# Performance work log

Measured on AMD Instinct MI355X. Metric: run time of the kernel, lower is better.

Reference implementation:

```python
import jax, jax.numpy as jnp
import numpy as np

H = 768
R = 24


def setup_inputs() -> dict:
    key = jax.random.key(0)
    ks = jax.random.split(key, 9)
    B, S = 4, 256
    hidden = jax.random.normal(ks[0], (B, S, H), dtype=jnp.float32)
    # ConcatHandshaking fc: Linear(2H -> H); torch weight shape (out,in)=(H,2H)
    fc_w = jax.random.normal(ks[1], (H, 2 * H), dtype=jnp.float32) * (1.0 / np.sqrt(2 * H))
    fc_b = jnp.zeros((H,), dtype=jnp.float32)
    # h2t: Linear(H -> 2)
    h2t_w = jax.random.normal(ks[2], (2, H), dtype=jnp.float32) * (1.0 / np.sqrt(H))
    h2t_b = jnp.zeros((2,), dtype=jnp.float32)
    # h2h / t2t TaggingProjector: R independent Linear(H -> 3), batched as (R,3,H)
    h2h_w = jax.random.normal(ks[3], (R, 3, H), dtype=jnp.float32) * (1.0 / np.sqrt(H))
    h2h_b = jnp.zeros((R, 3), dtype=jnp.float32)
    t2t_w = jax.random.normal(ks[4], (R, 3, H), dtype=jnp.float32) * (1.0 / np.sqrt(H))
    t2t_b = jnp.zeros((R, 3), dtype=jnp.float32)
    return {
        "hidden": hidden,
        "fc_w": fc_w, "fc_b": fc_b,
        "h2t_w": h2t_w, "h2t_b": h2t_b,
        "h2h_w": h2h_w, "h2h_b": h2h_b,
        "t2t_w": t2t_w, "t2t_b": t2t_b,
    }


def _handshaking(hidden, fc_w, fc_b):
    # hidden: (B, S, H). Pairs (i, j) with i <= j in row-major (torch loop) order.
    S = hidden.shape[1]
    idx_i, idx_j = jnp.triu_indices(S)  # each (P,), P = S(S+1)/2
    # concat([h_i, h_j]) @ W^T == h_i @ Wl^T + h_j @ Wr^T  (avoids (B,P,2H) buffer)
    Wl = fc_w[:, :H]  # (H, H)
    Wr = fc_w[:, H:]  # (H, H)
    left = jnp.einsum('bsh,oh->bso', hidden, Wl)   # (B, S, H)
    right = jnp.einsum('bsh,oh->bso', hidden, Wr)  # (B, S, H)
    hs = jnp.tanh(left[:, idx_i, :] + right[:, idx_j, :] + fc_b)  # (B, P, H)
    return hs


def reference(hidden, fc_w, fc_b, h2t_w, h2t_b, h2h_w, h2h_b, t2t_w, t2t_b):
    hs = _handshaking(hidden, fc_w, fc_b)  # (B, P, H)
    # h2t: plain Linear(H->2), logits (no softmax in original)
    h2t = jnp.einsum('bph,oh->bpo', hs, h2t_w) + h2t_b  # (B, P, 2)
    # TaggingProjector: batched per-relation Linear(H->3), then softmax over tags
    h2h = jax.nn.softmax(jnp.einsum('bph,rth->brpt', hs, h2h_w) + h2h_b[None, :, None, :], axis=-1)
    t2t = jax.nn.softmax(jnp.einsum('bph,rth->brpt', hs, t2t_w) + t2t_b[None, :, None, :], axis=-1)
    return (h2t, h2h, t2t)
```

## Files before the change

### kernel.cpp

```cpp
#include <hip/hip_runtime.h>
#include <hip/hip_bf16.h>

#define H 768
#define SEQ 256
#define NPAIR 32896
#define NOUTP 160
#define OFF_H2H 263168u
#define OFF_T2T 9737216u

#define N_BPK 122880
#define N_FCW 1179648

typedef short bf16x8 __attribute__((ext_vector_type(8)));
typedef float f32x4 __attribute__((ext_vector_type(4)));

__device__ __forceinline__ float tanh_act(float x) {
    float e = __builtin_amdgcn_exp2f(x * 2.8853900817779268f);
    return fmaf(-2.0f, __builtin_amdgcn_rcpf(e + 1.0f), 1.0f);
}
__device__ __forceinline__ float bf_lo(int w){ return __uint_as_float(((unsigned)w) << 16); }
__device__ __forceinline__ float bf_hi(int w){ return __uint_as_float(((unsigned)w) & 0xffff0000u); }
__device__ __forceinline__ int cvtpk(float lo, float hi) {
    int r;
    asm("v_cvt_pk_bf16_f32 %0, %1, %2" : "=v"(r) : "v"(lo), "v"(hi));
    return r;
}
__device__ __forceinline__ unsigned short bf16r(float x){
    unsigned int u = __float_as_uint(x);
    u += 0x7fffu + ((u >> 16) & 1u);
    return (unsigned short)(u >> 16);
}

__device__ __forceinline__ int row_start(int i) { return i * SEQ - (i * (i - 1)) / 2; }
__device__ __forceinline__ void pair_ij(int p, int& oi, int& oj) {
    double disc = 263169.0 - 8.0 * (double)p;
    int i = (int)((513.0 - sqrt(disc)) * 0.5);
    if (i > 0 && row_start(i) > p) --i;
    while (row_start(i + 1) <= p) ++i;
    oi = i;
    oj = i + (p - row_start(i));
}

__global__ __launch_bounds__(256) void pack_kernel(
    const float* __restrict__ h2t_w, const float* __restrict__ h2h_w,
    const float* __restrict__ t2t_w, const float* __restrict__ h2t_b,
    const float* __restrict__ h2h_b, const float* __restrict__ t2t_b,
    const float* __restrict__ fc_w,
    unsigned short* __restrict__ Bpk, unsigned short* __restrict__ fcwb,
    float* __restrict__ bc)
{
    int idx = blockIdx.x * 256 + threadIdx.x;
    if (idx < N_BPK) {
        int j = idx & 7, lane = (idx >> 3) & 63, rest = idx >> 9;
        int f = rest % 10, k32 = rest / 10;
        int n = f * 16 + (lane & 15);
        int k = k32 * 32 + ((lane >> 4) << 3) + j;
        float v = 0.f;
        if (n < 2)        v = h2t_w[n * H + k];
        else if (n < 74)  v = h2h_w[(n - 2) * H + k];
        else if (n < 146) v = t2t_w[(n - 74) * H + k];
        Bpk[idx] = bf16r(v);
    } else if (idx < N_BPK + N_FCW) {
        int q = idx - N_BPK;
        int n = q / H, k = q % H;
        float v = (n < H) ? fc_w[(size_t)n * 2 * H + k]
                          : fc_w[(size_t)(n - H) * 2 * H + H + k];
        fcwb[q] = bf16r(v);
    } else if (idx < N_BPK + N_FCW + NOUTP) {
        int q = idx - N_BPK - N_FCW;
        float v = 0.f;
        if (q < 2)        v = h2t_b[q];
        else if (q < 74)  v = h2h_b[q - 2];
        else if (q < 146) v = t2t_b[q - 74];
        bc[q] = v;
    }
}

__global__ __launch_bounds__(256, 2) void lr_mfma(
    const float* __restrict__ hidden, const unsigned short* __restrict__ fcwb,
    const float* __restrict__ fc_b,
    unsigned short* __restrict__ LB, unsigned short* __restrict__ RB)
{
    __shared__ __align__(16) char sm[24576];
    const int tid = threadIdx.x, l = tid & 63, w = tid >> 6;
    const int wm = w >> 1, wn = w & 1;
    const int m0 = blockIdx.x * 64, n0 = blockIdx.y * 128;
    f32x4 acc[2][4] = {};
    for (int c = 0; c < 12; ++c) {
        const int k0 = c * 64;
        #pragma unroll
        for (int it = 0; it < 2; ++it) {
            int idx = tid + it * 256;
            int row = idx >> 3, k8 = idx & 7;
            const float4* src = reinterpret_cast<const float4*>(hidden + (size_t)(m0 + row) * H + k0 + k8 * 8);
            float4 a = src[0], bq = src[1];
            int4 st;
            st.x = cvtpk(a.x, a.y);  st.y = cvtpk(a.z, a.w);
            st.z = cvtpk(bq.x, bq.y); st.w = cvtpk(bq.z, bq.w);
            *reinterpret_cast<int4*>(sm + row * 128 + ((k8 * 16) ^ ((row & 7) << 4))) = st;
        }
        #pragma unroll
        for (int it = 0; it < 4; ++it) {
            int idx = tid + it * 256;
            int row = idx >> 3, k8 = idx & 7;
            *reinterpret_cast<int4*>(sm + 8192 + row * 128 + ((k8 * 16) ^ ((row & 7) << 4))) =
                *reinterpret_cast<const int4*>(fcwb + (size_t)(n0 + row) * H + k0 + k8 * 8);
        }
        __syncthreads();
        #pragma unroll
        for (int kk = 0; kk < 2; ++kk) {
            const int sl = kk * 4 + (l >> 4);
            const int swz = (l & 7) << 4;
            bf16x8 af[2], bfr[4];
            #pragma unroll
            for (int a = 0; a < 2; ++a) {
                int row = 32 * wm + 16 * a + (l & 15);
                af[a] = *reinterpret_cast<const bf16x8*>(sm + row * 128 + ((sl * 16) ^ swz));
            }
            #pragma unroll
            for (int f = 0; f < 4; ++f) {
                int row = 64 * wn + 16 * f + (l & 15);
                bfr[f] = *reinterpret_cast<const bf16x8*>(sm + 8192 + row * 128 + ((sl * 16) ^ swz));
            }
            #pragma unroll
            for (int a = 0; a < 2; ++a)
                #pragma unroll
                for (int f = 0; f < 4; ++f)
                    acc[a][f] = __builtin_amdgcn_mfma_f32_16x16x32_bf16(af[a], bfr[f], acc[a][f], 0, 0, 0);
        }
        __syncthreads();
    }
    #pragma unroll
    for (int a = 0; a < 2; ++a)
        #pragma unroll
        for (int f = 0; f < 4; ++f)
            #pragma unroll
            for (int r = 0; r < 4; ++r) {
                int row = m0 + 32 * wm + 16 * a + 4 * (l >> 4) + r;
                int col = n0 + 64 * wn + 16 * f + (l & 15);
                float v = acc[a][f][r];
                if (n0 < H) LB[(size_t)row * H + col] = bf16r(v + fc_b[col]);
                else        RB[(size_t)row * H + (col - H)] = bf16r(v);
            }
}

__device__ __forceinline__ void stage_row(char* dst, const unsigned short* lp, const unsigned short* rp) {
    int4 lv = *reinterpret_cast<const int4*>(lp);
    int4 rv = *reinterpret_cast<const int4*>(rp);
    int4 st;
    st.x = cvtpk(tanh_act(bf_lo(lv.x) + bf_lo(rv.x)), tanh_act(bf_hi(lv.x) + bf_hi(rv.x)));
    st.y = cvtpk(tanh_act(bf_lo(lv.y) + bf_lo(rv.y)), tanh_act(bf_hi(lv.y) + bf_hi(rv.y)));
    st.z = cvtpk(tanh_act(bf_lo(lv.z) + bf_lo(rv.z)), tanh_act(bf_hi(lv.z) + bf_hi(rv.z)));
    st.w = cvtpk(tanh_act(bf_lo(lv.w) + bf_lo(rv.w)), tanh_act(bf_hi(lv.w) + bf_hi(rv.w)));
    *reinterpret_cast<int4*>(dst) = st;
}

__global__ __launch_bounds__(512, 4) void pair_mfma(
    const unsigned short* __restrict__ LB, const unsigned short* __restrict__ RB,
    const unsigned short* __restrict__ Bpk, const float* __restrict__ bc,
    float* __restrict__ out)
{
    __shared__ __align__(16) char sm[38528];
    int*   iOf  = reinterpret_cast<int*>(sm + 36864);
    int*   jOf  = reinterpret_cast<int*>(sm + 37376);
    float* bc_s = reinterpret_cast<float*>(sm + 37888);

    const int tid = threadIdx.x, l = tid & 63, w = tid >> 6;
    const int wm = w >> 1, wn = w & 1;
    const int b = blockIdx.y, p0 = blockIdx.x * 128;

    if (tid < 128) {
        int i, j; pair_ij(p0 + tid, i, j);
        iOf[tid] = i * H; jOf[tid] = j * H;
    }
    if (tid < NOUTP) bc_s[tid] = bc[tid];
    __syncthreads();

    const unsigned short* LBb = LB + (size_t)b * SEQ * H;
    const unsigned short* RBb = RB + (size_t)b * SEQ * H;
    const int qA = tid >> 3, k8 = tid & 7;
    const unsigned short* lpA = LBb + iOf[qA] + k8 * 8;
    const unsigned short* rpA = RBb + jOf[qA] + k8 * 8;
    const unsigned short* lpB = LBb + iOf[qA + 64] + k8 * 8;
    const unsigned short* rpB = RBb + jOf[qA + 64] + k8 * 8;
    char* stA = sm + qA * 128 + ((k8 * 16) ^ ((qA & 7) << 4));
    char* stB = stA + 64 * 128;

    f32x4 acc[2][5] = {};
    const int4* bsrc = reinterpret_cast<const int4*>(Bpk);
    int4* bdst = reinterpret_cast<int4*>(sm + 16384);

    for (int c = 0; c < 12; ++c) {
        const int k0 = c * 64;
        stage_row(stA, lpA + k0, rpA + k0);
        stage_row(stB, lpB + k0, rpB + k0);
        bdst[tid]        = bsrc[c * 1280 + tid];
        bdst[tid + 512]  = bsrc[c * 1280 + tid + 512];
        if (tid < 256) bdst[tid + 1024] = bsrc[c * 1280 + tid + 1024];
        __syncthreads();
        #pragma unroll
        for (int kk = 0; kk < 2; ++kk) {
            const int sl16 = (kk * 4 + (l >> 4)) * 16;
            const int swz = (l & 7) << 4;
            bf16x8 af[2];
            #pragma unroll
            for (int m = 0; m < 2; ++m) {
                int row = 32 * wm + 16 * m + (l & 15);
                af[m] = *reinterpret_cast<const bf16x8*>(sm + row * 128 + (sl16 ^ swz));
            }
            #pragma unroll
            for (int f = 0; f < 5; ++f) {
                bf16x8 bfr = *reinterpret_cast<const bf16x8*>(
                    sm + 16384 + ((kk * 10 + wn * 5 + f) * 64 + l) * 16);
                #pragma unroll
                for (int m = 0; m < 2; ++m)
                    acc[m][f] = __builtin_amdgcn_mfma_f32_16x16x32_bf16(af[m], bfr, acc[m][f], 0, 0, 0);
            }
        }
        __syncthreads();
    }

    float* scw = reinterpret_cast<float*>(sm);
    for (int s = 0; s < 4; ++s) {
        if (wm == s) {
            #pragma unroll
            for (int m = 0; m < 2; ++m)
                #pragma unroll
                for (int f = 0; f < 5; ++f)
                    #pragma unroll
                    for (int r = 0; r < 4; ++r) {
                        int rl = 16 * m + 4 * (l >> 4) + r;
                        int col = 80 * wn + 16 * f + (l & 15);
                        scw[rl * 172 + col] = acc[m][f][r];
                    }
        }
        __syncthreads();
        if (tid < 64) {
            int rl = tid >> 1, tt = tid & 1;
            int p = p0 + 32 * s + rl;
            out[((size_t)b * NPAIR + p) * 2 + tt] = scw[rl * 172 + tt] + bc_s[tt];
        }
        #pragma unroll
        for (int it = 0; it < 3; ++it) {
            int item = it * 512 + tid;
            int rl = item & 31, rr = item >> 5;
            int ob = 2 + rr * 3;
            float l0 = scw[rl * 172 + ob + 0] + bc_s[ob + 0];
            float l1 = scw[rl * 172 + ob + 1] + bc_s[ob + 1];
            float l2 = scw[rl * 172 + ob + 2] + bc_s[ob + 2];
            float mx = fmaxf(l0, fmaxf(l1, l2));
            float e0 = __expf(l0 - mx), e1 = __expf(l1 - mx), e2 = __expf(l2 - mx);
            float inv = __fdividef(1.0f, e0 + e1 + e2);
            int p = p0 + 32 * s + rl;
            size_t base = (rr < 24)
                ? (size_t)OFF_H2H + ((size_t)(b * 24 + rr) * NPAIR + p) * 3
                : (size_t)OFF_T2T + ((size_t)(b * 24 + rr - 24) * NPAIR + p) * 3;
            out[base + 0] = e0 * inv;
            out[base + 1] = e1 * inv;
            out[base + 2] = e2 * inv;
        }
        __syncthreads();
    }
}

extern "C" void kernel_launch(void* const* d_in, const int* in_sizes, int n_in,
                              void* d_out, int out_size, void* d_ws, size_t ws_size,
                              hipStream_t stream) {
    const float* hidden = (const float*)d_in[0];
    const float* fc_w   = (const float*)d_in[1];
    const float* fc_b   = (const float*)d_in[2];
    const float* h2t_w  = (const float*)d_in[3];
    const float* h2t_b  = (const float*)d_in[4];
    const float* h2h_w  = (const float*)d_in[5];
    const float* h2h_b  = (const float*)d_in[6];
    const float* t2t_w  = (const float*)d_in[7];
    const float* t2t_b  = (const float*)d_in[8];

    char* wsb = (char*)d_ws;
    unsigned short* LBw  = (unsigned short*)(wsb);
    unsigned short* RBw  = (unsigned short*)(wsb + 1572864);
    unsigned short* Bpk  = (unsigned short*)(wsb + 3145728);
    unsigned short* fcwb = (unsigned short*)(wsb + 3391488);
    float*          bc   = (float*)        (wsb + 5750784);

    float* out = (float*)d_out;

    pack_kernel<<<(N_BPK + N_FCW + NOUTP + 255) / 256, 256, 0, stream>>>(
        h2t_w, h2h_w, t2t_w, h2t_b, h2h_b, t2t_b, fc_w, Bpk, fcwb, bc);
    lr_mfma<<<dim3(16, 12), 256, 0, stream>>>(hidden, fcwb, fc_b, LBw, RBw);
    pair_mfma<<<dim3(NPAIR / 128, 4), 512, 0, stream>>>(LBw, RBw, Bpk, bc, out);
}
```

Before: 97.52 us.

## Double-buffer tanh staging and read B fragments directly from global

Restructures the pair kernel's K loop. The tanh-activated A tile is double-buffered in shared memory so the next chunk is loaded and activated while the current one feeds the MFMAs, leaving one barrier per iteration. The B weight fragments are now loaded straight from global into registers instead of being staged through LDS, and the exp2 scale factor is folded into the LB/RB epilogue of the first GEMM to drop one multiply per element. The cost is higher register pressure, with the occupancy hint removed from launch_bounds, plus repeated global or L2 reads of B by every wave and slightly different rounding from scaling before the bf16 conversion.

```diff
diff --git a/kernel.cpp b/kernel.cpp
--- a/kernel.cpp
+++ b/kernel.cpp
@@ -10,12 +10,13 @@
 
 #define N_BPK 122880
 #define N_FCW 1179648
+#define SCL 2.8853900817779268f
 
 typedef short bf16x8 __attribute__((ext_vector_type(8)));
 typedef float f32x4 __attribute__((ext_vector_type(4)));
 
-__device__ __forceinline__ float tanh_act(float x) {
-    float e = __builtin_amdgcn_exp2f(x * 2.8853900817779268f);
+__device__ __forceinline__ float tanh_s(float xs) {
+    float e = __builtin_amdgcn_exp2f(xs);
     return fmaf(-2.0f, __builtin_amdgcn_rcpf(e + 1.0f), 1.0f);
 }
 __device__ __forceinline__ float bf_lo(int w){ return __uint_as_float(((unsigned)w) << 16); }
@@ -29,6 +30,14 @@
     unsigned int u = __float_as_uint(x);
     u += 0x7fffu + ((u >> 16) & 1u);
     return (unsigned short)(u >> 16);
+}
+__device__ __forceinline__ int4 tanh_pack(int4 lv, int4 rv) {
+    int4 st;
+    st.x = cvtpk(tanh_s(bf_lo(lv.x) + bf_lo(rv.x)), tanh_s(bf_hi(lv.x) + bf_hi(rv.x)));
+    st.y = cvtpk(tanh_s(bf_lo(lv.y) + bf_lo(rv.y)), tanh_s(bf_hi(lv.y) + bf_hi(rv.y)));
+    st.z = cvtpk(tanh_s(bf_lo(lv.z) + bf_lo(rv.z)), tanh_s(bf_hi(lv.z) + bf_hi(rv.z)));
+    st.w = cvtpk(tanh_s(bf_lo(lv.w) + bf_lo(rv.w)), tanh_s(bf_hi(lv.w) + bf_hi(rv.w)));
+    return st;
 }
 
 __device__ __forceinline__ int row_start(int i) { return i * SEQ - (i * (i - 1)) / 2; }
@@ -139,31 +148,20 @@
                 int row = m0 + 32 * wm + 16 * a + 4 * (l >> 4) + r;
                 int col = n0 + 64 * wn + 16 * f + (l & 15);
                 float v = acc[a][f][r];
-                if (n0 < H) LB[(size_t)row * H + col] = bf16r(v + fc_b[col]);
-                else        RB[(size_t)row * H + (col - H)] = bf16r(v);
+                if (n0 < H) LB[(size_t)row * H + col] = bf16r((v + fc_b[col]) * SCL);
+                else        RB[(size_t)row * H + (col - H)] = bf16r(v * SCL);
             }
 }
 
-__device__ __forceinline__ void stage_row(char* dst, const unsigned short* lp, const unsigned short* rp) {
-    int4 lv = *reinterpret_cast<const int4*>(lp);
-    int4 rv = *reinterpret_cast<const int4*>(rp);
-    int4 st;
-    st.x = cvtpk(tanh_act(bf_lo(lv.x) + bf_lo(rv.x)), tanh_act(bf_hi(lv.x) + bf_hi(rv.x)));
-    st.y = cvtpk(tanh_act(bf_lo(lv.y) + bf_lo(rv.y)), tanh_act(bf_hi(lv.y) + bf_hi(rv.y)));
-    st.z = cvtpk(tanh_act(bf_lo(lv.z) + bf_lo(rv.z)), tanh_act(bf_hi(lv.z) + bf_hi(rv.z)));
-    st.w = cvtpk(tanh_act(bf_lo(lv.w) + bf_lo(rv.w)), tanh_act(bf_hi(lv.w) + bf_hi(rv.w)));
-    *reinterpret_cast<int4*>(dst) = st;
-}
-
-__global__ __launch_bounds__(512, 4) void pair_mfma(
+__global__ __launch_bounds__(512) void pair_mfma(
     const unsigned short* __restrict__ LB, const unsigned short* __restrict__ RB,
     const unsigned short* __restrict__ Bpk, const float* __restrict__ bc,
     float* __restrict__ out)
 {
-    __shared__ __align__(16) char sm[38528];
-    int*   iOf  = reinterpret_cast<int*>(sm + 36864);
-    int*   jOf  = reinterpret_cast<int*>(sm + 37376);
-    float* bc_s = reinterpret_cast<float*>(sm + 37888);
+    __shared__ __align__(16) char sm[34432];
+    int*   iOf  = reinterpret_cast<int*>(sm + 32768);
+    int*   jOf  = reinterpret_cast<int*>(sm + 33280);
+    float* bc_s = reinterpret_cast<float*>(sm + 33792);
 
     const int tid = threadIdx.x, l = tid & 63, w = tid >> 6;
     const int wm = w >> 1, wn = w & 1;
@@ -183,39 +181,77 @@
     const unsigned short* rpA = RBb + jOf[qA] + k8 * 8;
     const unsigned short* lpB = LBb + iOf[qA + 64] + k8 * 8;
     const unsigned short* rpB = RBb + jOf[qA + 64] + k8 * 8;
-    char* stA = sm + qA * 128 + ((k8 * 16) ^ ((qA & 7) << 4));
-    char* stB = stA + 64 * 128;
+    const int stoff = qA * 128 + ((k8 * 16) ^ ((qA & 7) << 4));
+    const unsigned short* bqp = Bpk + wn * 2560 + l * 8;
 
     f32x4 acc[2][5] = {};
-    const int4* bsrc = reinterpret_cast<const int4*>(Bpk);
-    int4* bdst = reinterpret_cast<int4*>(sm + 16384);
+
+    {
+        int4 lA = *reinterpret_cast<const int4*>(lpA);
+        int4 rA = *reinterpret_cast<const int4*>(rpA);
+        int4 lB = *reinterpret_cast<const int4*>(lpB);
+        int4 rB = *reinterpret_cast<const int4*>(rpB);
+        *reinterpret_cast<int4*>(sm + stoff)        = tanh_pack(lA, rA);
+        *reinterpret_cast<int4*>(sm + stoff + 8192) = tanh_pack(lB, rB);
+    }
+    __syncthreads();
 
     for (int c = 0; c < 12; ++c) {
-        const int k0 = c * 64;
-        stage_row(stA, lpA + k0, rpA + k0);
-        stage_row(stB, lpB + k0, rpB + k0);
-        bdst[tid]        = bsrc[c * 1280 + tid];
-        bdst[tid + 512]  = bsrc[c * 1280 + tid + 512];
-        if (tid < 256) bdst[tid + 1024] = bsrc[c * 1280 + tid + 1024];
-        __syncthreads();
-        #pragma unroll
-        for (int kk = 0; kk < 2; ++kk) {
-            const int sl16 = (kk * 4 + (l >> 4)) * 16;
+        char* bufc = sm + ((c & 1) << 14);
+        char* bufn = sm + (((c + 1) & 1) << 14);
+        const int off = (c < 11 ? (c + 1) : c) * 64;
+        int4 nlA = *reinterpret_cast<const int4*>(lpA + off);
+        int4 nrA = *reinterpret_cast<const int4*>(rpA + off);
+        int4 nlB = *reinterpret_cast<const int4*>(lpB + off);
+        int4 nrB = *reinterpret_cast<const int4*>(rpB + off);
+        const unsigned short* bqc = bqp + c * 10240;
+        bf16x8 bq0 = *reinterpret_cast<const bf16x8*>(bqc);
+        bf16x8 bq1 = *reinterpret_cast<const bf16x8*>(bqc + 512);
+        bf16x8 bq2 = *reinterpret_cast<const bf16x8*>(bqc + 1024);
+        bf16x8 bq3 = *reinterpret_cast<const bf16x8*>(bqc + 1536);
+        bf16x8 bq4 = *reinterpret_cast<const bf16x8*>(bqc + 2048);
+        if (c < 11) {
+            *reinterpret_cast<int4*>(bufn + stoff)        = tanh_pack(nlA, nrA);
+            *reinterpret_cast<int4*>(bufn + stoff + 8192) = tanh_pack(nlB, nrB);
+        }
+        bf16x8 bq5 = *reinterpret_cast<const bf16x8*>(bqc + 5120);
+        bf16x8 bq6 = *reinterpret_cast<const bf16x8*>(bqc + 5632);
+        bf16x8 bq7 = *reinterpret_cast<const bf16x8*>(bqc + 6144);
+        bf16x8 bq8 = *reinterpret_cast<const bf16x8*>(bqc + 6656);
+        bf16x8 bq9 = *reinterpret_cast<const bf16x8*>(bqc + 7168);
+        {
+            const int sl16 = (l >> 4) << 4;
             const int swz = (l & 7) << 4;
-            bf16x8 af[2];
-            #pragma unroll
-            for (int m = 0; m < 2; ++m) {
-                int row = 32 * wm + 16 * m + (l & 15);
-                af[m] = *reinterpret_cast<const bf16x8*>(sm + row * 128 + (sl16 ^ swz));
-            }
-            #pragma unroll
-            for (int f = 0; f < 5; ++f) {
-                bf16x8 bfr = *reinterpret_cast<const bf16x8*>(
-                    sm + 16384 + ((kk * 10 + wn * 5 + f) * 64 + l) * 16);
-                #pragma unroll
-                for (int m = 0; m < 2; ++m)
-                    acc[m][f] = __builtin_amdgcn_mfma_f32_16x16x32_bf16(af[m], bfr, acc[m][f], 0, 0, 0);
-            }
+            const int r0 = (32 * wm + (l & 15)) * 128;
+            bf16x8 af0 = *reinterpret_cast<const bf16x8*>(bufc + r0 + (sl16 ^ swz));
+            bf16x8 af1 = *reinterpret_cast<const bf16x8*>(bufc + r0 + 2048 + (sl16 ^ swz));
+            acc[0][0] = __builtin_amdgcn_mfma_f32_16x16x32_bf16(af0, bq0, acc[0][0], 0, 0, 0);
+            acc[1][0] = __builtin_amdgcn_mfma_f32_16x16x32_bf16(af1, bq0, acc[1][0], 0, 0, 0);
+            acc[0][1] = __builtin_amdgcn_mfma_f32_16x16x32_bf16(af0, bq1, acc[0][1], 0, 0, 0);
+            acc[1][1] = __builtin_amdgcn_mfma_f32_16x16x32_bf16(af1, bq1, acc[1][1], 0, 0, 0);
+            acc[0][2] = __builtin_amdgcn_mfma_f32_16x16x32_bf16(af0, bq2, acc[0][2], 0, 0, 0);
+            acc[1][2] = __builtin_amdgcn_mfma_f32_16x16x32_bf16(af1, bq2, acc[1][2], 0, 0, 0);
+            acc[0][3] = __builtin_amdgcn_mfma_f32_16x16x32_bf16(af0, bq3, acc[0][3], 0, 0, 0);
+            acc[1][3] = __builtin_amdgcn_mfma_f32_16x16x32_bf16(af1, bq3, acc[1][3], 0, 0, 0);
+            acc[0][4] = __builtin_amdgcn_mfma_f32_16x16x32_bf16(af0, bq4, acc[0][4], 0, 0, 0);
+            acc[1][4] = __builtin_amdgcn_mfma_f32_16x16x32_bf16(af1, bq4, acc[1][4], 0, 0, 0);
+        }
+        {
+            const int sl16 = (4 + (l >> 4)) << 4;
+            const int swz = (l & 7) << 4;
+            const int r0 = (32 * wm + (l & 15)) * 128;
+            bf16x8 af0 = *reinterpret_cast<const bf16x8*>(bufc + r0 + (sl16 ^ swz));
+            bf16x8 af1 = *reinterpret_cast<const bf16x8*>(bufc + r0 + 2048 + (sl16 ^ swz));
+            acc[0][0] = __builtin_amdgcn_mfma_f32_16x16x32_bf16(af0, bq5, acc[0][0], 0, 0, 0);
+            acc[1][0] = __builtin_amdgcn_mfma_f32_16x16x32_bf16(af1, bq5, acc[1][0], 0, 0, 0);
+            acc[0][1] = __builtin_amdgcn_mfma_f32_16x16x32_bf16(af0, bq6, acc[0][1], 0, 0, 0);
+            acc[1][1] = __builtin_amdgcn_mfma_f32_16x16x32_bf16(af1, bq6, acc[1][1], 0, 0, 0);
+            acc[0][2] = __builtin_amdgcn_mfma_f32_16x16x32_bf16(af0, bq7, acc[0][2], 0, 0, 0);
+            acc[1][2] = __builtin_amdgcn_mfma_f32_16x16x32_bf16(af1, bq7, acc[1][2], 0, 0, 0);
+            acc[0][3] = __builtin_amdgcn_mfma_f32_16x16x32_bf16(af0, bq8, acc[0][3], 0, 0, 0);
+            acc[1][3] = __builtin_amdgcn_mfma_f32_16x16x32_bf16(af1, bq8, acc[1][3], 0, 0, 0);
+            acc[0][4] = __builtin_amdgcn_mfma_f32_16x16x32_bf16(af0, bq9, acc[0][4], 0, 0, 0);
+            acc[1][4] = __builtin_amdgcn_mfma_f32_16x16x32_bf16(af1, bq9, acc[1][4], 0, 0, 0);
         }
         __syncthreads();
     }
```

Result: slower. 110.7 us (+13.6%).

## Compute tanh A-fragments in registers and double-buffer B weights in pair kernel

Applied to the files above, without the earlier changes.

The pair kernel now runs 256 threads with each wave owning 32 rows and all 160 output columns. The tanh of L+R is computed straight into MFMA A-fragments in registers, so the A tile is no longer staged through shared memory. The B weight tiles are double-buffered in LDS with register prefetch, and the next chunk's global loads overlap the MFMAs, which removes one barrier per iteration. The tanh scale factor is folded into the LR kernel's bf16 outputs, saving a multiply per element, at the cost of slightly different rounding, higher register pressure (20 accumulators) and lower occupancy.

```diff
diff --git a/kernel.cpp b/kernel.cpp
--- a/kernel.cpp
+++ b/kernel.cpp
@@ -10,12 +10,13 @@
 
 #define N_BPK 122880
 #define N_FCW 1179648
+#define SCL 2.8853900817779268f
 
 typedef short bf16x8 __attribute__((ext_vector_type(8)));
 typedef float f32x4 __attribute__((ext_vector_type(4)));
 
-__device__ __forceinline__ float tanh_act(float x) {
-    float e = __builtin_amdgcn_exp2f(x * 2.8853900817779268f);
+__device__ __forceinline__ float tanh_s(float xs) {
+    float e = __builtin_amdgcn_exp2f(xs);
     return fmaf(-2.0f, __builtin_amdgcn_rcpf(e + 1.0f), 1.0f);
 }
 __device__ __forceinline__ float bf_lo(int w){ return __uint_as_float(((unsigned)w) << 16); }
@@ -29,6 +30,14 @@
     unsigned int u = __float_as_uint(x);
     u += 0x7fffu + ((u >> 16) & 1u);
     return (unsigned short)(u >> 16);
+}
+__device__ __forceinline__ bf16x8 tanh_frag(int4 lv, int4 rv) {
+    int4 st;
+    st.x = cvtpk(tanh_s(bf_lo(lv.x) + bf_lo(rv.x)), tanh_s(bf_hi(lv.x) + bf_hi(rv.x)));
+    st.y = cvtpk(tanh_s(bf_lo(lv.y) + bf_lo(rv.y)), tanh_s(bf_hi(lv.y) + bf_hi(rv.y)));
+    st.z = cvtpk(tanh_s(bf_lo(lv.z) + bf_lo(rv.z)), tanh_s(bf_hi(lv.z) + bf_hi(rv.z)));
+    st.w = cvtpk(tanh_s(bf_lo(lv.w) + bf_lo(rv.w)), tanh_s(bf_hi(lv.w) + bf_hi(rv.w)));
+    return __builtin_bit_cast(bf16x8, st);
 }
 
 __device__ __forceinline__ int row_start(int i) { return i * SEQ - (i * (i - 1)) / 2; }
@@ -139,34 +148,22 @@
                 int row = m0 + 32 * wm + 16 * a + 4 * (l >> 4) + r;
                 int col = n0 + 64 * wn + 16 * f + (l & 15);
                 float v = acc[a][f][r];
-                if (n0 < H) LB[(size_t)row * H + col] = bf16r(v + fc_b[col]);
-                else        RB[(size_t)row * H + (col - H)] = bf16r(v);
+                if (n0 < H) LB[(size_t)row * H + col] = bf16r((v + fc_b[col]) * SCL);
+                else        RB[(size_t)row * H + (col - H)] = bf16r(v * SCL);
             }
 }
 
-__device__ __forceinline__ void stage_row(char* dst, const unsigned short* lp, const unsigned short* rp) {
-    int4 lv = *reinterpret_cast<const int4*>(lp);
-    int4 rv = *reinterpret_cast<const int4*>(rp);
-    int4 st;
-    st.x = cvtpk(tanh_act(bf_lo(lv.x) + bf_lo(rv.x)), tanh_act(bf_hi(lv.x) + bf_hi(rv.x)));
-    st.y = cvtpk(tanh_act(bf_lo(lv.y) + bf_lo(rv.y)), tanh_act(bf_hi(lv.y) + bf_hi(rv.y)));
-    st.z = cvtpk(tanh_act(bf_lo(lv.z) + bf_lo(rv.z)), tanh_act(bf_hi(lv.z) + bf_hi(rv.z)));
-    st.w = cvtpk(tanh_act(bf_lo(lv.w) + bf_lo(rv.w)), tanh_act(bf_hi(lv.w) + bf_hi(rv.w)));
-    *reinterpret_cast<int4*>(dst) = st;
-}
-
-__global__ __launch_bounds__(512, 4) void pair_mfma(
+__global__ __launch_bounds__(256, 3) void pair_mfma(
     const unsigned short* __restrict__ LB, const unsigned short* __restrict__ RB,
     const unsigned short* __restrict__ Bpk, const float* __restrict__ bc,
     float* __restrict__ out)
 {
-    __shared__ __align__(16) char sm[38528];
-    int*   iOf  = reinterpret_cast<int*>(sm + 36864);
-    int*   jOf  = reinterpret_cast<int*>(sm + 37376);
-    float* bc_s = reinterpret_cast<float*>(sm + 37888);
+    __shared__ __align__(16) char sm[42624];
+    int*   iOf  = reinterpret_cast<int*>(sm + 40960);
+    int*   jOf  = reinterpret_cast<int*>(sm + 41472);
+    float* bc_s = reinterpret_cast<float*>(sm + 41984);
 
     const int tid = threadIdx.x, l = tid & 63, w = tid >> 6;
-    const int wm = w >> 1, wn = w & 1;
     const int b = blockIdx.y, p0 = blockIdx.x * 128;
 
     if (tid < 128) {
@@ -178,60 +175,101 @@
 
     const unsigned short* LBb = LB + (size_t)b * SEQ * H;
     const unsigned short* RBb = RB + (size_t)b * SEQ * H;
-    const int qA = tid >> 3, k8 = tid & 7;
-    const unsigned short* lpA = LBb + iOf[qA] + k8 * 8;
-    const unsigned short* rpA = RBb + jOf[qA] + k8 * 8;
-    const unsigned short* lpB = LBb + iOf[qA + 64] + k8 * 8;
-    const unsigned short* rpB = RBb + jOf[qA + 64] + k8 * 8;
-    char* stA = sm + qA * 128 + ((k8 * 16) ^ ((qA & 7) << 4));
-    char* stB = stA + 64 * 128;
-
-    f32x4 acc[2][5] = {};
+    const int row0 = 32 * w + (l & 15);
+    const int kb = (l >> 4) << 3;
+    const unsigned short* lp0 = LBb + iOf[row0] + kb;
+    const unsigned short* rp0 = RBb + jOf[row0] + kb;
+    const unsigned short* lp1 = LBb + iOf[row0 + 16] + kb;
+    const unsigned short* rp1 = RBb + jOf[row0 + 16] + kb;
+
     const int4* bsrc = reinterpret_cast<const int4*>(Bpk);
-    int4* bdst = reinterpret_cast<int4*>(sm + 16384);
-
-    for (int c = 0; c < 12; ++c) {
-        const int k0 = c * 64;
-        stage_row(stA, lpA + k0, rpA + k0);
-        stage_row(stB, lpB + k0, rpB + k0);
-        bdst[tid]        = bsrc[c * 1280 + tid];
-        bdst[tid + 512]  = bsrc[c * 1280 + tid + 512];
-        if (tid < 256) bdst[tid + 1024] = bsrc[c * 1280 + tid + 1024];
-        __syncthreads();
-        #pragma unroll
-        for (int kk = 0; kk < 2; ++kk) {
-            const int sl16 = (kk * 4 + (l >> 4)) * 16;
-            const int swz = (l & 7) << 4;
-            bf16x8 af[2];
-            #pragma unroll
-            for (int m = 0; m < 2; ++m) {
-                int row = 32 * wm + 16 * m + (l & 15);
-                af[m] = *reinterpret_cast<const bf16x8*>(sm + row * 128 + (sl16 ^ swz));
-            }
-            #pragma unroll
-            for (int f = 0; f < 5; ++f) {
-                bf16x8 bfr = *reinterpret_cast<const bf16x8*>(
-                    sm + 16384 + ((kk * 10 + wn * 5 + f) * 64 + l) * 16);
-                #pragma unroll
-                for (int m = 0; m < 2; ++m)
-                    acc[m][f] = __builtin_amdgcn_mfma_f32_16x16x32_bf16(af[m], bfr, acc[m][f], 0, 0, 0);
-            }
-        }
-        __syncthreads();
-    }
+    f32x4 acc[2][10] = {};
+
+    int4 nb0 = bsrc[tid], nb1 = bsrc[tid + 256], nb2 = bsrc[tid + 512],
+         nb3 = bsrc[tid + 768], nb4 = bsrc[tid + 1024];
+    int4 lA0 = *reinterpret_cast<const int4*>(lp0);
+    int4 lA1 = *reinterpret_cast<const int4*>(lp0 + 32);
+    int4 lB0 = *reinterpret_cast<const int4*>(lp1);
+    int4 lB1 = *reinterpret_cast<const int4*>(lp1 + 32);
+    int4 rA0 = *reinterpret_cast<const int4*>(rp0);
+    int4 rA1 = *reinterpret_cast<const int4*>(rp0 + 32);
+    int4 rB0 = *reinterpret_cast<const int4*>(rp1);
+    int4 rB1 = *reinterpret_cast<const int4*>(rp1 + 32);
+    {
+        int4* bw = reinterpret_cast<int4*>(sm);
+        bw[tid] = nb0; bw[tid + 256] = nb1; bw[tid + 512] = nb2;
+        bw[tid + 768] = nb3; bw[tid + 1024] = nb4;
+    }
+    __syncthreads();
+
+    #pragma unroll 2
+    for (int c = 0; c < 11; ++c) {
+        const int4* bn = bsrc + (c + 1) * 1280;
+        nb0 = bn[tid]; nb1 = bn[tid + 256]; nb2 = bn[tid + 512];
+        nb3 = bn[tid + 768]; nb4 = bn[tid + 1024];
+        bf16x8 a00 = tanh_frag(lA0, rA0);
+        bf16x8 a10 = tanh_frag(lB0, rB0);
+        bf16x8 a01 = tanh_frag(lA1, rA1);
+        bf16x8 a11 = tanh_frag(lB1, rB1);
+        const int co = (c + 1) * 64;
+        lA0 = *reinterpret_cast<const int4*>(lp0 + co);
+        lA1 = *reinterpret_cast<const int4*>(lp0 + co + 32);
+        lB0 = *reinterpret_cast<const int4*>(lp1 + co);
+        lB1 = *reinterpret_cast<const int4*>(lp1 + co + 32);
+        rA0 = *reinterpret_cast<const int4*>(rp0 + co);
+        rA1 = *reinterpret_cast<const int4*>(rp0 + co + 32);
+        rB0 = *reinterpret_cast<const int4*>(rp1 + co);
+        rB1 = *reinterpret_cast<const int4*>(rp1 + co + 32);
+        const char* bufc = sm + ((c & 1) ? 20480 : 0);
+        #pragma unroll
+        for (int f = 0; f < 10; ++f) {
+            bf16x8 bf0 = *reinterpret_cast<const bf16x8*>(bufc + (f * 64 + l) * 16);
+            acc[0][f] = __builtin_amdgcn_mfma_f32_16x16x32_bf16(a00, bf0, acc[0][f], 0, 0, 0);
+            acc[1][f] = __builtin_amdgcn_mfma_f32_16x16x32_bf16(a10, bf0, acc[1][f], 0, 0, 0);
+        }
+        #pragma unroll
+        for (int f = 0; f < 10; ++f) {
+            bf16x8 bf1 = *reinterpret_cast<const bf16x8*>(bufc + ((10 + f) * 64 + l) * 16);
+            acc[0][f] = __builtin_amdgcn_mfma_f32_16x16x32_bf16(a01, bf1, acc[0][f], 0, 0, 0);
+            acc[1][f] = __builtin_amdgcn_mfma_f32_16x16x32_bf16(a11, bf1, acc[1][f], 0, 0, 0);
+        }
+        int4* bufn = reinterpret_cast<int4*>(sm + (((c + 1) & 1) ? 20480 : 0));
+        bufn[tid] = nb0; bufn[tid + 256] = nb1; bufn[tid + 512] = nb2;
+        bufn[tid + 768] = nb3; bufn[tid + 1024] = nb4;
+        __syncthreads();
+    }
+    {
+        bf16x8 a00 = tanh_frag(lA0, rA0);
+        bf16x8 a10 = tanh_frag(lB0, rB0);
+        bf16x8 a01 = tanh_frag(lA1, rA1);
+        bf16x8 a11 = tanh_frag(lB1, rB1);
+        const char* bufc = sm + 20480;
+        #pragma unroll
+        for (int f = 0; f < 10; ++f) {
+            bf16x8 bf0 = *reinterpret_cast<const bf16x8*>(bufc + (f * 64 + l) * 16);
+            acc[0][f] = __builtin_amdgcn_mfma_f32_16x16x32_bf16(a00, bf0, acc[0][f], 0, 0, 0);
+            acc[1][f] = __builtin_amdgcn_mfma_f32_16x16x32_bf16(a10, bf0, acc[1][f], 0, 0, 0);
+        }
+        #pragma unroll
+        for (int f = 0; f < 10; ++f) {
+            bf16x8 bf1 = *reinterpret_cast<const bf16x8*>(bufc + ((10 + f) * 64 + l) * 16);
+            acc[0][f] = __builtin_amdgcn_mfma_f32_16x16x32_bf16(a01, bf1, acc[0][f], 0, 0, 0);
+            acc[1][f] = __builtin_amdgcn_mfma_f32_16x16x32_bf16(a11, bf1, acc[1][f], 0, 0, 0);
+        }
+    }
+    __syncthreads();
 
     float* scw = reinterpret_cast<float*>(sm);
     for (int s = 0; s < 4; ++s) {
-        if (wm == s) {
+        if (w == s) {
             #pragma unroll
             for (int m = 0; m < 2; ++m)
                 #pragma unroll
-                for (int f = 0; f < 5; ++f)
+                for (int f = 0; f < 10; ++f)
                     #pragma unroll
                     for (int r = 0; r < 4; ++r) {
                         int rl = 16 * m + 4 * (l >> 4) + r;
-                        int col = 80 * wn + 16 * f + (l & 15);
-                        scw[rl * 172 + col] = acc[m][f][r];
+                        scw[rl * 172 + f * 16 + (l & 15)] = acc[m][f][r];
                     }
         }
         __syncthreads();
@@ -241,8 +279,8 @@
             out[((size_t)b * NPAIR + p) * 2 + tt] = scw[rl * 172 + tt] + bc_s[tt];
         }
         #pragma unroll
-        for (int it = 0; it < 3; ++it) {
-            int item = it * 512 + tid;
+        for (int it = 0; it < 6; ++it) {
+            int item = it * 256 + tid;
             int rl = item & 31, rr = item >> 5;
             int ob = 2 + rr * 3;
             float l0 = scw[rl * 172 + ob + 0] + bc_s[ob + 0];
@@ -288,5 +326,5 @@
     pack_kernel<<<(N_BPK + N_FCW + NOUTP + 255) / 256, 256, 0, stream>>>(
         h2t_w, h2h_w, t2t_w, h2t_b, h2h_b, t2t_b, fc_w, Bpk, fcwb, bc);
     lr_mfma<<<dim3(16, 12), 256, 0, stream>>>(hidden, fcwb, fc_b, LBw, RBw);
-    pair_mfma<<<dim3(NPAIR / 128, 4), 512, 0, stream>>>(LBw, RBw, Bpk, bc, out);
-}
+    pair_mfma<<<dim3(NPAIR / 128, 4), 256, 0, stream>>>(LBw, RBw, Bpk, bc, out);
+}
```

Result: no change. 96.47 us (-1.1%).
